# Performance work log

Measured on AMD Instinct MI355X. Metric: run time of the kernel, lower is better.

Reference implementation:

```python
import jax, jax.numpy as jnp
import numpy as np
import math

PHI = (1.0 + math.sqrt(5.0)) / 2.0
TWO_PI = 2.0 * math.pi

V, D, L, N, RES = 50257, 128, 2, 256, 4096
B, S = 2, 512

# global sin/cos lookup tables over [0, 2*pi), matching get_global_lut(lut_resolution)
_grid = jnp.arange(RES, dtype=jnp.float32) * (TWO_PI / RES)
SIN_T = jnp.sin(_grid)
COS_T = jnp.cos(_grid)


def lut_sin_cos(theta):
    # quantize phase to table index (Python-style mod keeps result non-negative)
    idx = jnp.floor(theta * (RES / TWO_PI)).astype(jnp.int32) % RES
    return SIN_T[idx], COS_T[idx]


def setup_inputs() -> dict:
    key = jax.random.key(0)
    ks = jax.random.split(key, 10)
    xav_c = 0.5 * math.sqrt(2.0 / (2 * D + D))   # xavier gain=0.5 for input_collapse
    xav_o = 0.5 * math.sqrt(2.0 / (N + D))       # xavier for out_proj
    xav_v = 0.5 * math.sqrt(2.0 / (D + V))       # xavier for ComplexLinear
    return {
        "input_ids": jax.random.randint(ks[0], (B, S), 0, V),
        "emb": jax.random.normal(ks[1], (V, 2 * D), jnp.float32) * (0.02 * 0.5),
        "cw": jax.random.normal(ks[2], (L, D, 2 * D), jnp.float32) * xav_c,
        "cb": jnp.zeros((L, D), jnp.float32),
        "W": jax.random.normal(ks[3], (L, N, D), jnp.float32) * 0.02,
        "Bp": jnp.zeros((L, N, D), jnp.float32),
        "attn_cos": jnp.ones((L, N, D), jnp.float32),
        "attn_sin": jnp.ones((L, N, D), jnp.float32),
        "opr": jax.random.normal(ks[4], (L, D, N), jnp.float32) * xav_o,
        "opi": jax.random.normal(ks[5], (L, D, N), jnp.float32) * xav_o,
        "Wr": jax.random.normal(ks[6], (V, D), jnp.float32) * xav_v,
        "Wi": jax.random.normal(ks[7], (V, D), jnp.float32) * xav_v,
    }


def reference(input_ids, emb, cw, cb, W, Bp, attn_cos, attn_sin, opr, opi, Wr, Wi):
    e = emb[input_ids]                         # (B,S,2D) token embedding
    xr, xi = e[..., :D], e[..., D:]            # complex hidden state parts
    t = (jnp.arange(S, dtype=jnp.float32) * PHI)[None, :, None, None]  # golden-ratio timesteps
    for l in range(L):
        xc = jnp.concatenate([xr, xi], axis=-1) @ cw[l].T + cb[l]      # (B,S,D) input collapse
        wavelength = 1.0 + jnp.abs(W[l])                               # (N,D)
        theta = xc[:, :, None, :] / wavelength + Bp[l] + t             # (B,S,N,D)
        s, c = lut_sin_cos(theta)
        cos_sum = jnp.einsum('bsnd,nd->bsn', c, attn_cos[l])           # interference sums
        sin_sum = jnp.einsum('bsnd,nd->bsn', s, attn_sin[l])
        xr = jax.nn.silu(cos_sum @ opr[l].T)                           # (B,S,D)
        xi = jax.nn.silu(sin_sum @ opi[l].T)
    # ComplexLinear output projection (no bias), then collapse to real logits via magnitude
    lr = xr @ Wr.T - xi @ Wi.T
    li = xi @ Wr.T + xr @ Wi.T
    return jnp.sqrt(lr * lr + li * li + 1e-8)  # (B,S,V)
```

## Files before the change

### kernel.cpp

```cpp
#include <hip/hip_runtime.h>
#include <math.h>

#define VV 50257
#define Dm 128
#define NN 256
#define RESN 4096
#define SEQ 512
#define TOK 1024

using f32x4_t = __attribute__((ext_vector_type(4))) float;
using s16x8_t = __attribute__((ext_vector_type(8))) short;
using u16x4_t = __attribute__((ext_vector_type(4))) unsigned short;

static __device__ __forceinline__ unsigned short f2bf(float f) {
    unsigned u = __builtin_bit_cast(unsigned, f);
    u += 0x7fffu + ((u >> 16) & 1u);
    return (unsigned short)(u >> 16);
}

static __device__ __forceinline__ void gload16(const unsigned short* g, unsigned short* l) {
    __builtin_amdgcn_global_load_lds(
        (const __attribute__((address_space(1))) unsigned int*)g,
        (__attribute__((address_space(3))) unsigned int*)l, 16, 0, 0);
}

__global__ void pack_kernel(const float* __restrict__ W, const float* __restrict__ Bp,
                            const float* __restrict__ ac, const float* __restrict__ as_,
                            const float* __restrict__ cw, const float* __restrict__ opr,
                            const float* __restrict__ opi,
                            float4* __restrict__ packed, float* __restrict__ cwT,
                            float* __restrict__ oprT, float* __restrict__ opiT,
                            float2* __restrict__ lutg) {
    int tid = blockIdx.x * 256 + threadIdx.x;
    int l = tid >> 15;
    int rem = tid & 32767;
    {
        int d = rem >> 8, n = rem & 255;
        int src = (l * NN + n) * Dm + d;
        float4 pk;
        pk.x = 1.0f / (1.0f + fabsf(W[src]));
        pk.y = Bp[src];
        pk.z = ac[src];
        pk.w = as_[src];
        packed[tid] = pk;
    }
    {
        int k = rem >> 7, d = rem & 127;
        cwT[tid] = cw[(l * Dm + d) * (2 * Dm) + k];
    }
    {
        int n = rem >> 7, d = rem & 127;
        oprT[tid] = opr[(l * Dm + d) * NN + n];
        opiT[tid] = opi[(l * Dm + d) * NN + n];
    }
    if (tid < RESN) {
        float ang = (float)tid * (float)(6.283185307179586476925286766559 / 4096.0);
        lutg[tid] = make_float2(sinf(ang), cosf(ang));
    }
}

__global__ void wconv_kernel(const float* __restrict__ Wr, const float* __restrict__ Wi,
                             unsigned short* __restrict__ Wr_bf,
                             unsigned short* __restrict__ Wi_bf) {
    int gid = blockIdx.x * 256 + threadIdx.x;
    int base = gid * 4;
    if (base < VV * Dm) {
        float4 r = *(const float4*)(Wr + base);
        float4 w = *(const float4*)(Wi + base);
        *(u16x4_t*)(Wr_bf + base) = (u16x4_t){f2bf(r.x), f2bf(r.y), f2bf(r.z), f2bf(r.w)};
        *(u16x4_t*)(Wi_bf + base) = (u16x4_t){f2bf(w.x), f2bf(w.y), f2bf(w.z), f2bf(w.w)};
    }
}

__global__ void embed_kernel(const int* __restrict__ ids, const float* __restrict__ emb,
                             float* __restrict__ x) {
    int t = blockIdx.x;
    int k = threadIdx.x;
    x[t * 256 + k] = emb[(size_t)ids[t] * 256 + k];
}

__global__ void xc_kernel(const float* __restrict__ x, const float* __restrict__ cwT,
                          const float* __restrict__ cb, float* __restrict__ xc, int l) {
    __shared__ float xs[2][256];
    int tid = threadIdx.x;
    int t0 = blockIdx.x * 2;
    xs[0][tid] = x[t0 * 256 + tid];
    xs[1][tid] = x[(t0 + 1) * 256 + tid];
    __syncthreads();
    int j = tid >> 7, d = tid & 127;
    const float* cwb = cwT + l * 32768;
    float acc = 0.f;
#pragma unroll 8
    for (int k = 0; k < 256; k++) acc = fmaf(xs[j][k], cwb[k * 128 + d], acc);
    xc[(t0 + j) * 128 + d] = acc + cb[l * 128 + d];
}

__global__ void __launch_bounds__(256) theta_kernel(const float* __restrict__ xc,
                                                    const float4* __restrict__ packed,
                                                    const float2* __restrict__ lutg,
                                                    float* __restrict__ pr_part,
                                                    float* __restrict__ pi_part, int l) {
    __shared__ float2 lut[RESN];
    __shared__ float xcs[4][64];
    int tid = threadIdx.x;
    int t0 = blockIdx.x * 4;
    int dh = blockIdx.y;
    const float4* lg = (const float4*)lutg;
    float4* ldst = (float4*)lut;
#pragma unroll
    for (int i = 0; i < 8; i++) ldst[tid + i * 256] = lg[tid + i * 256];
    {
        int j = tid >> 6, i = tid & 63;
        xcs[j][i] = xc[(t0 + j) * 128 + dh * 64 + i];
    }
    __syncthreads();
    float tv[4];
#pragma unroll
    for (int j = 0; j < 4; j++) {
        int s = (t0 + j) & (SEQ - 1);
        tv[j] = (float)s * 1.61803398874989485f;
    }
    const float4* pk = packed + ((size_t)(l * Dm + dh * 64)) * NN + tid;
    float cs[4] = {0, 0, 0, 0}, sn[4] = {0, 0, 0, 0};
    const float SC = (float)(4096.0 / 6.283185307179586476925286766559);
    for (int d = 0; d < 64; d++) {
        float4 p = pk[(size_t)d * NN];
#pragma unroll
        for (int j = 0; j < 4; j++) {
            float th = fmaf(xcs[j][d], p.x, p.y) + tv[j];
            int idx = ((int)floorf(th * SC)) & (RESN - 1);
            float2 scv = lut[idx];
            cs[j] = fmaf(scv.y, p.z, cs[j]);
            sn[j] = fmaf(scv.x, p.w, sn[j]);
        }
    }
#pragma unroll
    for (int j = 0; j < 4; j++) {
        pr_part[(size_t)(dh * TOK + t0 + j) * NN + tid] = cs[j];
        pi_part[(size_t)(dh * TOK + t0 + j) * NN + tid] = sn[j];
    }
}

__global__ void proj_kernel(const float* __restrict__ pr_part, const float* __restrict__ pi_part,
                            const float* __restrict__ oprT, const float* __restrict__ opiT,
                            float* __restrict__ x, unsigned short* __restrict__ x_bf, int l) {
    __shared__ float prs[4][256], pis[4][256];
    int tid = threadIdx.x;
    int t0 = blockIdx.x * 4;
#pragma unroll
    for (int i = 0; i < 4; i++) {
        prs[i][tid] = pr_part[(size_t)(t0 + i) * 256 + tid] +
                      pr_part[(size_t)(TOK + t0 + i) * 256 + tid];
        pis[i][tid] = pi_part[(size_t)(t0 + i) * 256 + tid] +
                      pi_part[(size_t)(TOK + t0 + i) * 256 + tid];
    }
    __syncthreads();
    int g = tid >> 7, d = tid & 127;
    const float* wb = (g == 0 ? oprT : opiT) + l * 32768;
    const float(*ps)[256] = (g == 0) ? prs : pis;
    float acc[4] = {0, 0, 0, 0};
    for (int n = 0; n < 256; n++) {
        float wv = wb[n * 128 + d];
#pragma unroll
        for (int j = 0; j < 4; j++) acc[j] = fmaf(ps[j][n], wv, acc[j]);
    }
#pragma unroll
    for (int j = 0; j < 4; j++) {
        float v = acc[j];
        float s = v / (1.0f + expf(-v));
        x[(t0 + j) * 256 + g * 128 + d] = s;
        x_bf[(t0 + j) * 256 + g * 128 + d] = f2bf(s);
    }
}

__global__ void __launch_bounds__(256, 2) final_kernel(const unsigned short* __restrict__ x_bf,
                                                       const unsigned short* __restrict__ Wr_bf,
                                                       const unsigned short* __restrict__ Wi_bf,
                                                       float* __restrict__ out) {
    __shared__ unsigned short lds[2][12288];
    int tid = threadIdx.x;
    int wg = blockIdx.x;
    int wp = (wg & 7) * 786 + (wg >> 3);
    int vb = wp >> 3, tb = wp & 7;
    int v0 = vb * 64, t0 = tb * 128;

    int wv = tid >> 6, lane = tid & 63;
    int wm = wv >> 1, wn = wv & 1;
    int quad = lane >> 4, t16 = lane & 15;

    int r_loc = lane >> 2;
    int csw = (lane & 3) ^ ((lane >> 3) & 3);
    const unsigned short* srcA0 = x_bf + (size_t)(t0 + 32 * wv + r_loc) * 256 + csw * 8;
    const unsigned short* srcA1 = srcA0 + 16 * 256;
    int vv_ = v0 + 16 * wv + r_loc;
    if (vv_ > VV - 1) vv_ = VV - 1;
    const unsigned short* srcWr = Wr_bf + (size_t)vv_ * 128 + csw * 8;
    const unsigned short* srcWi = Wi_bf + (size_t)vv_ * 128 + csw * 8;

    int rsw = (t16 >> 1) & 3;
    int rdA = (wm * 64 + t16) * 32 + ((quad ^ rsw) << 3);
    int rdB = (wn * 32 + t16) * 32 + ((quad ^ rsw) << 3);

    f32x4_t aRR[4][2], aII[4][2], aIR[4][2], aRI[4][2];
#pragma unroll
    for (int im = 0; im < 4; im++)
#pragma unroll
        for (int in = 0; in < 2; in++) {
            aRR[im][in] = (f32x4_t){0.f, 0.f, 0.f, 0.f};
            aII[im][in] = (f32x4_t){0.f, 0.f, 0.f, 0.f};
            aIR[im][in] = (f32x4_t){0.f, 0.f, 0.f, 0.f};
            aRI[im][in] = (f32x4_t){0.f, 0.f, 0.f, 0.f};
        }

#define STAGE(b, kc)                                                             \
    {                                                                            \
        const int ko = (kc) * 32;                                                \
        unsigned short* bb = lds[(b)];                                           \
        gload16(srcA0 + ko, bb + wv * 1024);                                     \
        gload16(srcA1 + ko, bb + wv * 1024 + 512);                               \
        gload16(srcA0 + 128 + ko, bb + 4096 + wv * 1024);                        \
        gload16(srcA1 + 128 + ko, bb + 4096 + wv * 1024 + 512);                  \
        gload16(srcWr + ko, bb + 8192 + wv * 512);                               \
        gload16(srcWi + ko, bb + 10240 + wv * 512);                              \
    }

    STAGE(0, 0);
#pragma unroll
    for (int kc = 0; kc < 4; kc++) {
        if (kc < 3) {
            STAGE((kc + 1) & 1, kc + 1);
            asm volatile("s_waitcnt vmcnt(6)" ::: "memory");
        } else {
            asm volatile("s_waitcnt vmcnt(0)" ::: "memory");
        }
        __builtin_amdgcn_s_barrier();
        __builtin_amdgcn_sched_barrier(0);
        const unsigned short* B = lds[kc & 1];
        s16x8_t ar[4], ai[4], fr[2], fi[2];
#pragma unroll
        for (int im = 0; im < 4; im++) {
            ar[im] = *(const s16x8_t*)(B + rdA + im * 512);
            ai[im] = *(const s16x8_t*)(B + 4096 + rdA + im * 512);
        }
#pragma unroll
        for (int in = 0; in < 2; in++) {
            fr[in] = *(const s16x8_t*)(B + 8192 + rdB + in * 512);
            fi[in] = *(const s16x8_t*)(B + 10240 + rdB + in * 512);
        }
#pragma unroll
        for (int im = 0; im < 4; im++)
#pragma unroll
            for (int in = 0; in < 2; in++) {
                aRR[im][in] = __builtin_amdgcn_mfma_f32_16x16x32_bf16(ar[im], fr[in],
                                                                      aRR[im][in], 0, 0, 0);
                aII[im][in] = __builtin_amdgcn_mfma_f32_16x16x32_bf16(ai[im], fi[in],
                                                                      aII[im][in], 0, 0, 0);
                aIR[im][in] = __builtin_amdgcn_mfma_f32_16x16x32_bf16(ai[im], fr[in],
                                                                      aIR[im][in], 0, 0, 0);
                aRI[im][in] = __builtin_amdgcn_mfma_f32_16x16x32_bf16(ar[im], fi[in],
                                                                      aRI[im][in], 0, 0, 0);
            }
        __builtin_amdgcn_s_barrier();
    }
#undef STAGE

#pragma unroll
    for (int im = 0; im < 4; im++) {
        int trow = t0 + wm * 64 + im * 16 + quad * 4;
#pragma unroll
        for (int in = 0; in < 2; in++) {
            int v = v0 + wn * 32 + in * 16 + t16;
            if (v < VV) {
#pragma unroll
                for (int r = 0; r < 4; r++) {
                    float lr = aRR[im][in][r] - aII[im][in][r];
                    float li = aIR[im][in][r] + aRI[im][in][r];
                    out[(size_t)(trow + r) * VV + v] = sqrtf(fmaf(lr, lr, fmaf(li, li, 1e-8f)));
                }
            }
        }
    }
}

extern "C" void kernel_launch(void* const* d_in, const int* in_sizes, int n_in,
                              void* d_out, int out_size, void* d_ws, size_t ws_size,
                              hipStream_t stream) {
    const int* ids   = (const int*)d_in[0];
    const float* emb = (const float*)d_in[1];
    const float* cw  = (const float*)d_in[2];
    const float* cb  = (const float*)d_in[3];
    const float* W   = (const float*)d_in[4];
    const float* Bp  = (const float*)d_in[5];
    const float* ac  = (const float*)d_in[6];
    const float* as_ = (const float*)d_in[7];
    const float* opr = (const float*)d_in[8];
    const float* opi = (const float*)d_in[9];
    const float* Wr  = (const float*)d_in[10];
    const float* Wi  = (const float*)d_in[11];
    float* out = (float*)d_out;

    char* ws = (char*)d_ws;
    float*  x       = (float*)(ws);
    float*  xc      = (float*)(ws + (1u << 20));
    float*  pr_part = (float*)(ws + (2u << 20));
    float*  pi_part = (float*)(ws + (4u << 20));
    float4* packed  = (float4*)(ws + (6u << 20));
    float*  cwT     = (float*)(ws + (7u << 20));
    float*  oprT    = (float*)(ws + (7u << 20) + (256u << 10));
    float*  opiT    = (float*)(ws + (7u << 20) + (512u << 10));
    float2* lutg    = (float2*)(ws + (7u << 20) + (768u << 10));
    unsigned short* x_bf  = (unsigned short*)(ws + (8u  << 20));
    unsigned short* Wr_bf = (unsigned short*)(ws + (9u  << 20));
    unsigned short* Wi_bf = (unsigned short*)(ws + (22u << 20));

    pack_kernel<<<256, 256, 0, stream>>>(W, Bp, ac, as_, cw, opr, opi,
                                         packed, cwT, oprT, opiT, lutg);
    wconv_kernel<<<(VV * Dm / 4 + 255) / 256, 256, 0, stream>>>(Wr, Wi, Wr_bf, Wi_bf);
    embed_kernel<<<TOK, 256, 0, stream>>>(ids, emb, x);
    for (int l = 0; l < 2; l++) {
        xc_kernel<<<TOK / 2, 256, 0, stream>>>(x, cwT, cb, xc, l);
        theta_kernel<<<dim3(TOK / 4, 2), 256, 0, stream>>>(xc, packed, lutg,
                                                           pr_part, pi_part, l);
        proj_kernel<<<TOK / 4, 256, 0, stream>>>(pr_part, pi_part, oprT, opiT, x, x_bf, l);
    }
    final_kernel<<<dim3(786 * 8), 256, 0, stream>>>(x_bf, Wr_bf, Wi_bf, out);
}
```

Measured before the change: 431.1 us.

## Fuse embed and both layers into one mid kernel; deepen final GEMM prefetch

Replaces the embed, xc, theta and proj kernels (seven launches) with one mid_kernel that handles two tokens per block across both layers. Intermediates stay in shared memory and the LUT is loaded once per block, removing global round-trips and launch gaps. In exchange, each block does the full 128-d theta loop for only two tokens, and there are fewer blocks (512). The final GEMM also issues the first two k-chunk stages up front and refills buffers after each barrier, changing how loads are prefetched.

```diff
diff --git a/kernel.cpp b/kernel.cpp
--- a/kernel.cpp
+++ b/kernel.cpp
@@ -72,105 +72,88 @@
     }
 }
 
-__global__ void embed_kernel(const int* __restrict__ ids, const float* __restrict__ emb,
-                             float* __restrict__ x) {
-    int t = blockIdx.x;
-    int k = threadIdx.x;
-    x[t * 256 + k] = emb[(size_t)ids[t] * 256 + k];
-}
-
-__global__ void xc_kernel(const float* __restrict__ x, const float* __restrict__ cwT,
-                          const float* __restrict__ cb, float* __restrict__ xc, int l) {
+__global__ void __launch_bounds__(256) mid_kernel(const int* __restrict__ ids,
+                                                  const float* __restrict__ emb,
+                                                  const float* __restrict__ cwT,
+                                                  const float* __restrict__ cb,
+                                                  const float4* __restrict__ packed,
+                                                  const float2* __restrict__ lutg,
+                                                  const float* __restrict__ oprT,
+                                                  const float* __restrict__ opiT,
+                                                  unsigned short* __restrict__ x_bf) {
+    __shared__ float2 lut[RESN];
     __shared__ float xs[2][256];
+    __shared__ float xcp[2][2][128];
+    __shared__ float xc_s[2][128];
+    __shared__ float cs_s[2][256], sn_s[2][256];
+
     int tid = threadIdx.x;
     int t0 = blockIdx.x * 2;
-    xs[0][tid] = x[t0 * 256 + tid];
-    xs[1][tid] = x[(t0 + 1) * 256 + tid];
-    __syncthreads();
-    int j = tid >> 7, d = tid & 127;
-    const float* cwb = cwT + l * 32768;
-    float acc = 0.f;
-#pragma unroll 8
-    for (int k = 0; k < 256; k++) acc = fmaf(xs[j][k], cwb[k * 128 + d], acc);
-    xc[(t0 + j) * 128 + d] = acc + cb[l * 128 + d];
-}
-
-__global__ void __launch_bounds__(256) theta_kernel(const float* __restrict__ xc,
-                                                    const float4* __restrict__ packed,
-                                                    const float2* __restrict__ lutg,
-                                                    float* __restrict__ pr_part,
-                                                    float* __restrict__ pi_part, int l) {
-    __shared__ float2 lut[RESN];
-    __shared__ float xcs[4][64];
-    int tid = threadIdx.x;
-    int t0 = blockIdx.x * 4;
-    int dh = blockIdx.y;
+
     const float4* lg = (const float4*)lutg;
     float4* ldst = (float4*)lut;
 #pragma unroll
     for (int i = 0; i < 8; i++) ldst[tid + i * 256] = lg[tid + i * 256];
-    {
-        int j = tid >> 6, i = tid & 63;
-        xcs[j][i] = xc[(t0 + j) * 128 + dh * 64 + i];
-    }
+#pragma unroll
+    for (int j = 0; j < 2; j++) xs[j][tid] = emb[(size_t)ids[t0 + j] * 256 + tid];
     __syncthreads();
-    float tv[4];
-#pragma unroll
-    for (int j = 0; j < 4; j++) {
-        int s = (t0 + j) & (SEQ - 1);
-        tv[j] = (float)s * 1.61803398874989485f;
-    }
-    const float4* pk = packed + ((size_t)(l * Dm + dh * 64)) * NN + tid;
-    float cs[4] = {0, 0, 0, 0}, sn[4] = {0, 0, 0, 0};
+
+    int h = tid >> 7, d = tid & 127;
+    float tv[2];
+#pragma unroll
+    for (int j = 0; j < 2; j++) tv[j] = (float)((t0 + j) & (SEQ - 1)) * 1.61803398874989485f;
     const float SC = (float)(4096.0 / 6.283185307179586476925286766559);
-    for (int d = 0; d < 64; d++) {
-        float4 p = pk[(size_t)d * NN];
-#pragma unroll
-        for (int j = 0; j < 4; j++) {
-            float th = fmaf(xcs[j][d], p.x, p.y) + tv[j];
-            int idx = ((int)floorf(th * SC)) & (RESN - 1);
-            float2 scv = lut[idx];
-            cs[j] = fmaf(scv.y, p.z, cs[j]);
-            sn[j] = fmaf(scv.x, p.w, sn[j]);
-        }
-    }
-#pragma unroll
-    for (int j = 0; j < 4; j++) {
-        pr_part[(size_t)(dh * TOK + t0 + j) * NN + tid] = cs[j];
-        pi_part[(size_t)(dh * TOK + t0 + j) * NN + tid] = sn[j];
-    }
-}
-
-__global__ void proj_kernel(const float* __restrict__ pr_part, const float* __restrict__ pi_part,
-                            const float* __restrict__ oprT, const float* __restrict__ opiT,
-                            float* __restrict__ x, unsigned short* __restrict__ x_bf, int l) {
-    __shared__ float prs[4][256], pis[4][256];
-    int tid = threadIdx.x;
-    int t0 = blockIdx.x * 4;
-#pragma unroll
-    for (int i = 0; i < 4; i++) {
-        prs[i][tid] = pr_part[(size_t)(t0 + i) * 256 + tid] +
-                      pr_part[(size_t)(TOK + t0 + i) * 256 + tid];
-        pis[i][tid] = pi_part[(size_t)(t0 + i) * 256 + tid] +
-                      pi_part[(size_t)(TOK + t0 + i) * 256 + tid];
-    }
-    __syncthreads();
-    int g = tid >> 7, d = tid & 127;
-    const float* wb = (g == 0 ? oprT : opiT) + l * 32768;
-    const float(*ps)[256] = (g == 0) ? prs : pis;
-    float acc[4] = {0, 0, 0, 0};
-    for (int n = 0; n < 256; n++) {
-        float wv = wb[n * 128 + d];
-#pragma unroll
-        for (int j = 0; j < 4; j++) acc[j] = fmaf(ps[j][n], wv, acc[j]);
-    }
-#pragma unroll
-    for (int j = 0; j < 4; j++) {
-        float v = acc[j];
-        float s = v / (1.0f + expf(-v));
-        x[(t0 + j) * 256 + g * 128 + d] = s;
-        x_bf[(t0 + j) * 256 + g * 128 + d] = f2bf(s);
-    }
+
+    for (int l = 0; l < 2; l++) {
+        const float* cwb = cwT + l * 32768;
+#pragma unroll
+        for (int j = 0; j < 2; j++) {
+            float acc = 0.f;
+#pragma unroll 8
+            for (int k = h * 128; k < h * 128 + 128; k++)
+                acc = fmaf(xs[j][k], cwb[k * 128 + d], acc);
+            xcp[j][h][d] = acc;
+        }
+        __syncthreads();
+        xc_s[h][d] = xcp[h][0][d] + xcp[h][1][d] + cb[l * 128 + d];
+        __syncthreads();
+        const float4* pk = packed + (size_t)(l * Dm) * NN + tid;
+        float cs[2] = {0, 0}, sn[2] = {0, 0};
+        for (int dd = 0; dd < 128; dd++) {
+            float4 p = pk[(size_t)dd * NN];
+#pragma unroll
+            for (int j = 0; j < 2; j++) {
+                float th = fmaf(xc_s[j][dd], p.x, p.y) + tv[j];
+                int idx = ((int)floorf(th * SC)) & (RESN - 1);
+                float2 scv = lut[idx];
+                cs[j] = fmaf(scv.y, p.z, cs[j]);
+                sn[j] = fmaf(scv.x, p.w, sn[j]);
+            }
+        }
+#pragma unroll
+        for (int j = 0; j < 2; j++) {
+            cs_s[j][tid] = cs[j];
+            sn_s[j][tid] = sn[j];
+        }
+        __syncthreads();
+        const float* wb = (h == 0 ? oprT : opiT) + l * 32768;
+        const float(*ps)[256] = (h == 0) ? cs_s : sn_s;
+        float acc[2] = {0, 0};
+        for (int n = 0; n < 256; n++) {
+            float wv = wb[n * 128 + d];
+#pragma unroll
+            for (int j = 0; j < 2; j++) acc[j] = fmaf(ps[j][n], wv, acc[j]);
+        }
+        __syncthreads();
+#pragma unroll
+        for (int j = 0; j < 2; j++) {
+            float v = acc[j];
+            xs[j][tid] = v / (1.0f + expf(-v));
+        }
+        __syncthreads();
+    }
+#pragma unroll
+    for (int j = 0; j < 2; j++) x_bf[(size_t)(t0 + j) * 256 + tid] = f2bf(xs[j][tid]);
 }
 
 __global__ void __launch_bounds__(256, 2) final_kernel(const unsigned short* __restrict__ x_bf,
@@ -225,10 +208,10 @@
     }
 
     STAGE(0, 0);
+    STAGE(1, 1);
 #pragma unroll
     for (int kc = 0; kc < 4; kc++) {
         if (kc < 3) {
-            STAGE((kc + 1) & 1, kc + 1);
             asm volatile("s_waitcnt vmcnt(6)" ::: "memory");
         } else {
             asm volatile("s_waitcnt vmcnt(0)" ::: "memory");
@@ -261,6 +244,7 @@
                                                                       aRI[im][in], 0, 0, 0);
             }
         __builtin_amdgcn_s_barrier();
+        if (kc < 2) STAGE(kc & 1, kc + 2);
     }
 #undef STAGE
 
@@ -300,10 +284,6 @@
     float* out = (float*)d_out;
 
     char* ws = (char*)d_ws;
-    float*  x       = (float*)(ws);
-    float*  xc      = (float*)(ws + (1u << 20));
-    float*  pr_part = (float*)(ws + (2u << 20));
-    float*  pi_part = (float*)(ws + (4u << 20));
     float4* packed  = (float4*)(ws + (6u << 20));
     float*  cwT     = (float*)(ws + (7u << 20));
     float*  oprT    = (float*)(ws + (7u << 20) + (256u << 10));
@@ -316,12 +296,7 @@
     pack_kernel<<<256, 256, 0, stream>>>(W, Bp, ac, as_, cw, opr, opi,
                                          packed, cwT, oprT, opiT, lutg);
     wconv_kernel<<<(VV * Dm / 4 + 255) / 256, 256, 0, stream>>>(Wr, Wi, Wr_bf, Wi_bf);
-    embed_kernel<<<TOK, 256, 0, stream>>>(ids, emb, x);
-    for (int l = 0; l < 2; l++) {
-        xc_kernel<<<TOK / 2, 256, 0, stream>>>(x, cwT, cb, xc, l);
-        theta_kernel<<<dim3(TOK / 4, 2), 256, 0, stream>>>(xc, packed, lutg,
-                                                           pr_part, pi_part, l);
-        proj_kernel<<<TOK / 4, 256, 0, stream>>>(pr_part, pi_part, oprT, opiT, x, x_bf, l);
-    }
+    mid_kernel<<<TOK / 2, 256, 0, stream>>>(ids, emb, cwT, cb, packed, lutg,
+                                            oprT, opiT, x_bf);
     final_kernel<<<dim3(786 * 8), 256, 0, stream>>>(x_bf, Wr_bf, Wi_bf, out);
 }
```

Measured after the change: 420.3 us. -2.5%, faster.
